# Kernel optimization log

Measured on AMD Instinct MI355X. Metric: run time of the kernel, lower is better.

## Reference

```python
import jax, jax.numpy as jnp
import numpy as np

N = 4096  # nmentions
# Static index sets: strict lower triangle in row-major order (matches torch
# boolean-mask assignment order) and the diagonal.
ROWS, COLS = np.tril_indices(N, -1)
DIAG = np.arange(N)


def setup_inputs() -> dict:
    key = jax.random.key(0)
    k1, k2, k3 = jax.random.split(key, 3)
    eps_scores = jax.random.normal(k1, (N,), dtype=jnp.float32)
    ana_scores = jax.random.normal(k2, (N * (N - 1) // 2,), dtype=jnp.float32)
    # Build a coherent solution mask: random cluster ids; a mention's correct
    # antecedents are earlier mentions of the same cluster, else itself (epsilon).
    clusters = np.asarray(jax.random.randint(k3, (N,), 0, N // 8))
    same = clusters[:, None] == clusters[None, :]
    lower = np.tril(np.ones((N, N), dtype=bool), -1)
    sol_link = same & lower
    has_ante = sol_link.any(axis=1)
    mask = sol_link.astype(np.float32)
    mask[DIAG, DIAG] = (~has_ante).astype(np.float32)
    link_costs = jnp.array([[0.5], [1.0]], dtype=jnp.float32)  # [false_link],[wrong_link]
    false_new_cost = jnp.array([1.5], dtype=jnp.float32)
    return {
        "eps_scores": eps_scores,
        "ana_scores": ana_scores,
        "solution_mask": jnp.asarray(mask),
        "link_costs": link_costs,
        "false_new_cost": false_new_cost,
    }


def create_score_matrix(eps_scores, ana_scores):
    # [N,N]: diagonal = epsilon (non-anaphoric) scores, strict lower triangle =
    # pairwise antecedent scores in row-major tril order; upper triangle zero.
    scores = jnp.zeros((N, N), dtype=eps_scores.dtype)
    scores = scores.at[DIAG, DIAG].set(eps_scores)
    scores = scores.at[ROWS, COLS].set(ana_scores)
    return scores


def reference(eps_scores, ana_scores, solution_mask, link_costs, false_new_cost):
    scores = create_score_matrix(eps_scores, ana_scores)
    minimum_score = scores.min()
    solution_scores = solution_mask * scores + (1.0 - solution_mask) * minimum_score
    best_correct = solution_scores.max(axis=1)  # [N]
    non_anaphoric = jnp.diagonal(solution_mask)  # [N]
    # anaphoricity_selector @ link_costs.expand(2, N): each row is a constant
    # equal to false_link if non-anaphoric else wrong_link.
    row_cost = non_anaphoric * link_costs[0, 0] + (1.0 - non_anaphoric) * link_costs[1, 0]
    potential_costs = jnp.tril(jnp.broadcast_to(row_cost[:, None], (N, N)), -1)
    potential_costs = potential_costs.at[DIAG, DIAG].set(false_new_cost[0])
    cost_matrix = (1.0 - solution_mask) * potential_costs
    loss_values = cost_matrix * (1.0 + scores - best_correct[:, None])
    loss_per_example = loss_values.max(axis=1)  # [N]
    return loss_per_example
```

## Files before the change

### kernel.cpp

```cpp
#include <hip/hip_runtime.h>

#define N 4096
#define BLK 256
#define NEGF (-3.4e38f)

typedef float f4u __attribute__((ext_vector_type(4), aligned(4)));
typedef float f4a __attribute__((ext_vector_type(4), aligned(16)));

__global__ __launch_bounds__(BLK) void mention_loss_kernel(
    const float* __restrict__ eps_scores,
    const float* __restrict__ ana_scores,
    const float* __restrict__ mask,
    const float* __restrict__ link_costs,
    const float* __restrict__ false_new_cost,
    float* __restrict__ out)
{
    const int row = N - 1 - (int)blockIdx.x;
    const int tid = threadIdx.x;
    const long long base = (long long)row * (row - 1) / 2;
    const float* __restrict__ arow = ana_scores + base;
    const float* __restrict__ mrow = mask + (size_t)row * (size_t)N;

    float bc0 = NEGF, bc1 = NEGF, bc2 = NEGF, bc3 = NEGF;
    float sm0 = NEGF, sm1 = NEGF, sm2 = NEGF, sm3 = NEGF;

    int p = (int)((4 - (base & 3)) & 3);
    if (p > row) p = row;
    const int nvec = (row - p) >> 2;
    const int t0   = p + (nvec << 2);

#pragma unroll 4
    for (int g = tid; g < nvec; g += BLK) {
        const int j = p + (g << 2);
        const f4a s4 = *(const f4a*)(arow + j);
        const f4u m4 = *(const f4u*)(mrow + j);
        const bool o0 = (m4[0] != 0.0f);
        const bool o1 = (m4[1] != 0.0f);
        const bool o2 = (m4[2] != 0.0f);
        const bool o3 = (m4[3] != 0.0f);
        bc0 = fmaxf(bc0, o0 ? s4[0] : NEGF);
        sm0 = fmaxf(sm0, o0 ? NEGF : s4[0]);
        bc1 = fmaxf(bc1, o1 ? s4[1] : NEGF);
        sm1 = fmaxf(sm1, o1 ? NEGF : s4[1]);
        bc2 = fmaxf(bc2, o2 ? s4[2] : NEGF);
        sm2 = fmaxf(sm2, o2 ? NEGF : s4[2]);
        bc3 = fmaxf(bc3, o3 ? s4[3] : NEGF);
        sm3 = fmaxf(sm3, o3 ? NEGF : s4[3]);
    }
    if (tid < p) {
        const float s = arow[tid], m = mrow[tid];
        if (m != 0.0f) bc0 = fmaxf(bc0, s); else sm0 = fmaxf(sm0, s);
    }
    if (tid < row - t0) {
        const int j = t0 + tid;
        const float s = arow[j], m = mrow[j];
        if (m != 0.0f) bc1 = fmaxf(bc1, s); else sm1 = fmaxf(sm1, s);
    }
    float bc = fmaxf(fmaxf(bc0, bc1), fmaxf(bc2, bc3));
    float sm = fmaxf(fmaxf(sm0, sm1), fmaxf(sm2, sm3));

    for (int off = 32; off; off >>= 1) {
        bc = fmaxf(bc, __shfl_down(bc, off));
        sm = fmaxf(sm, __shfl_down(sm, off));
    }
    __shared__ float r_bc[BLK / 64], r_sm[BLK / 64];
    if ((tid & 63) == 0) { r_bc[tid >> 6] = bc; r_sm[tid >> 6] = sm; }
    __syncthreads();
    if (tid == 0) {
        float B = r_bc[0], S = r_sm[0];
#pragma unroll
        for (int w = 1; w < BLK / 64; ++w) {
            B = fmaxf(B, r_bc[w]);
            S = fmaxf(S, r_sm[w]);
        }
        const float e = eps_scores[row];
        const float d = mrow[row];
        if (d != 0.0f) B = fmaxf(B, e);
        const float rc = d * link_costs[0] + (1.0f - d) * link_costs[1];
        float loss = fmaxf(0.0f, rc * (1.0f + S - B));
        if (d == 0.0f) loss = fmaxf(loss, false_new_cost[0] * (1.0f + e - B));
        out[row] = loss;
    }
}

extern "C" void kernel_launch(void* const* d_in, const int* in_sizes, int n_in,
                              void* d_out, int out_size, void* d_ws, size_t ws_size,
                              hipStream_t stream) {
    const float* eps  = (const float*)d_in[0];
    const float* ana  = (const float*)d_in[1];
    const float* mask = (const float*)d_in[2];
    const float* lc   = (const float*)d_in[3];
    const float* fnc  = (const float*)d_in[4];
    float* out = (float*)d_out;

    mention_loss_kernel<<<N, BLK, 0, stream>>>(eps, ana, mask, lc, fnc, out);
}
```

Baseline: 117.2 us.

## Assign row pairs to single wavefronts to balance triangular work

Each row is now scanned by one 64-lane wavefront instead of a full 256-thread block. Each wave handles a long row (N-1-w) and its short partner (w) so every wave does about the same amount of triangular work, and the grid shrinks to N/8 blocks. This drops the shared-memory and __syncthreads block reduction in favour of a wave shuffle only. The cost is less parallelism per row and fewer waves in flight (2048 in total), which could limit how well memory latency is hidden.

Result: no change. 118.4 us (+1.0%).

```diff
diff --git a/kernel.cpp b/kernel.cpp
--- a/kernel.cpp
+++ b/kernel.cpp
@@ -7,16 +7,12 @@
 typedef float f4u __attribute__((ext_vector_type(4), aligned(4)));
 typedef float f4a __attribute__((ext_vector_type(4), aligned(16)));
 
-__global__ __launch_bounds__(BLK) void mention_loss_kernel(
-    const float* __restrict__ eps_scores,
+__device__ __forceinline__ void scan_row_wave(
     const float* __restrict__ ana_scores,
     const float* __restrict__ mask,
-    const float* __restrict__ link_costs,
-    const float* __restrict__ false_new_cost,
-    float* __restrict__ out)
+    const int row, const int lane,
+    float& bc_out, float& sm_out)
 {
-    const int row = N - 1 - (int)blockIdx.x;
-    const int tid = threadIdx.x;
     const long long base = (long long)row * (row - 1) / 2;
     const float* __restrict__ arow = ana_scores + base;
     const float* __restrict__ mrow = mask + (size_t)row * (size_t)N;
@@ -30,7 +26,7 @@
     const int t0   = p + (nvec << 2);
 
 #pragma unroll 4
-    for (int g = tid; g < nvec; g += BLK) {
+    for (int g = lane; g < nvec; g += 64) {
         const int j = p + (g << 2);
         const f4a s4 = *(const f4a*)(arow + j);
         const f4u m4 = *(const f4u*)(mrow + j);
@@ -47,39 +43,62 @@
         bc3 = fmaxf(bc3, o3 ? s4[3] : NEGF);
         sm3 = fmaxf(sm3, o3 ? NEGF : s4[3]);
     }
-    if (tid < p) {
-        const float s = arow[tid], m = mrow[tid];
+    if (lane < p) {
+        const float s = arow[lane], m = mrow[lane];
         if (m != 0.0f) bc0 = fmaxf(bc0, s); else sm0 = fmaxf(sm0, s);
     }
-    if (tid < row - t0) {
-        const int j = t0 + tid;
+    if (lane < row - t0) {
+        const int j = t0 + lane;
         const float s = arow[j], m = mrow[j];
         if (m != 0.0f) bc1 = fmaxf(bc1, s); else sm1 = fmaxf(sm1, s);
     }
-    float bc = fmaxf(fmaxf(bc0, bc1), fmaxf(bc2, bc3));
-    float sm = fmaxf(fmaxf(sm0, sm1), fmaxf(sm2, sm3));
+    bc_out = fmaxf(fmaxf(bc0, bc1), fmaxf(bc2, bc3));
+    sm_out = fmaxf(fmaxf(sm0, sm1), fmaxf(sm2, sm3));
+}
+
+__device__ __forceinline__ void epilogue(
+    const float* __restrict__ eps_scores,
+    const float* __restrict__ mask,
+    const float* __restrict__ link_costs,
+    const float* __restrict__ false_new_cost,
+    float* __restrict__ out,
+    const int row, float B, float S)
+{
+    const float e = eps_scores[row];
+    const float d = mask[(size_t)row * N + row];
+    if (d != 0.0f) B = fmaxf(B, e);
+    const float rc = d * link_costs[0] + (1.0f - d) * link_costs[1];
+    float loss = fmaxf(0.0f, rc * (1.0f + S - B));
+    if (d == 0.0f) loss = fmaxf(loss, false_new_cost[0] * (1.0f + e - B));
+    out[row] = loss;
+}
+
+__global__ __launch_bounds__(BLK) void mention_loss_kernel(
+    const float* __restrict__ eps_scores,
+    const float* __restrict__ ana_scores,
+    const float* __restrict__ mask,
+    const float* __restrict__ link_costs,
+    const float* __restrict__ false_new_cost,
+    float* __restrict__ out)
+{
+    const int lane = threadIdx.x & 63;
+    const int w    = ((int)blockIdx.x << 2) | (threadIdx.x >> 6);
+    const int rowA = N - 1 - w;
+    const int rowB = w;
+
+    float bcA, smA, bcB, smB;
+    scan_row_wave(ana_scores, mask, rowA, lane, bcA, smA);
+    scan_row_wave(ana_scores, mask, rowB, lane, bcB, smB);
 
     for (int off = 32; off; off >>= 1) {
-        bc = fmaxf(bc, __shfl_down(bc, off));
-        sm = fmaxf(sm, __shfl_down(sm, off));
+        bcA = fmaxf(bcA, __shfl_down(bcA, off));
+        smA = fmaxf(smA, __shfl_down(smA, off));
+        bcB = fmaxf(bcB, __shfl_down(bcB, off));
+        smB = fmaxf(smB, __shfl_down(smB, off));
     }
-    __shared__ float r_bc[BLK / 64], r_sm[BLK / 64];
-    if ((tid & 63) == 0) { r_bc[tid >> 6] = bc; r_sm[tid >> 6] = sm; }
-    __syncthreads();
-    if (tid == 0) {
-        float B = r_bc[0], S = r_sm[0];
-#pragma unroll
-        for (int w = 1; w < BLK / 64; ++w) {
-            B = fmaxf(B, r_bc[w]);
-            S = fmaxf(S, r_sm[w]);
-        }
-        const float e = eps_scores[row];
-        const float d = mrow[row];
-        if (d != 0.0f) B = fmaxf(B, e);
-        const float rc = d * link_costs[0] + (1.0f - d) * link_costs[1];
-        float loss = fmaxf(0.0f, rc * (1.0f + S - B));
-        if (d == 0.0f) loss = fmaxf(loss, false_new_cost[0] * (1.0f + e - B));
-        out[row] = loss;
+    if (lane == 0) {
+        epilogue(eps_scores, mask, link_costs, false_new_cost, out, rowA, bcA, smA);
+        epilogue(eps_scores, mask, link_costs, false_new_cost, out, rowB, bcB, smB);
     }
 }
 
@@ -93,5 +112,5 @@
     const float* fnc  = (const float*)d_in[4];
     float* out = (float*)d_out;
 
-    mention_loss_kernel<<<N, BLK, 0, stream>>>(eps, ana, mask, lc, fnc, out);
+    mention_loss_kernel<<<N / 8, BLK, 0, stream>>>(eps, ana, mask, lc, fnc, out);
 }
```
